# Kernel tuning notes

Hardware: AMD Instinct MI355X
Metric: run time of the kernel (lower is better)

## Reference

```python
import jax, jax.numpy as jnp
import numpy as np

NEG_BIG = -9e15  # matches -9000000000000000.0 in the torch source


def setup_inputs() -> dict:
    key = jax.random.key(0)
    k_h, k_adj, k_W, k_a = jax.random.split(key, 4)
    B, N, F_in, F_out = 8, 2048, 256, 256
    h = jax.random.normal(k_h, (B, N, F_in), dtype=jnp.float32)
    adj = jax.random.randint(k_adj, (B, N, N), 0, 2, dtype=jnp.int32)
    # xavier_uniform with gain=1.414
    gain = 1.414
    lim_W = gain * np.sqrt(6.0 / (F_in + F_out))
    W = jax.random.uniform(k_W, (F_in, F_out), dtype=jnp.float32, minval=-lim_W, maxval=lim_W)
    lim_a = gain * np.sqrt(6.0 / (2 * F_out + 1))
    a = jax.random.uniform(k_a, (2 * F_out, 1), dtype=jnp.float32, minval=-lim_a, maxval=lim_a)
    return {"h": h, "adj": adj, "W": W, "a": a}


def reference(h, adj, W, a):
    # h: [B, N, F_in], adj: [B, N, N], W: [F_in, F_out], a: [2*F_out, 1]
    F_out = W.shape[1]
    Wh = jnp.matmul(h, W)  # [B, N, F_out]
    a1 = a[:F_out, 0]      # [F_out]
    a2 = a[F_out:, 0]      # [F_out]
    # e_ij = Wh_i . a1 + Wh_j . a2  (identical to cat([Wh_i, Wh_j]) @ a)
    e = (Wh @ a1)[:, :, None] + (Wh @ a2)[:, None, :]  # [B, N, N]
    # NOTE: the original torch forward applies no LeakyReLU before softmax.
    masked = jnp.where(adj > 0, e, jnp.float32(NEG_BIG))
    attention = jax.nn.softmax(masked, axis=-1)  # [B, N, N]
    # dropout is a no-op in eval mode (training=False)
    h_prime = jnp.matmul(attention, Wh)  # [B, N, F_out]
    return jax.nn.elu(h_prime)
```

## Files before the change

### kernel.cpp

```cpp
#include <hip/hip_runtime.h>
#include <math.h>

using short8   = __attribute__((ext_vector_type(8))) short;
using floatx4  = __attribute__((ext_vector_type(4))) float;
using ushort4v = __attribute__((ext_vector_type(4))) unsigned short;

#define GLD16(gsrc, ldst) __builtin_amdgcn_global_load_lds( \
    (const __attribute__((address_space(1))) void*)(gsrc),  \
    (__attribute__((address_space(3))) void*)(ldst), 16, 0, 0)

__device__ __forceinline__ unsigned short f2bf(float x) {
  union { float f; unsigned u; } v; v.f = x;
  unsigned r = (v.u + 0x7FFFu + ((v.u >> 16) & 1u)) >> 16;
  return (unsigned short)r;
}
__device__ __forceinline__ float bf2f(unsigned short u) {
  union { unsigned u; float f; } v; v.u = ((unsigned)u) << 16;
  return v.f;
}
__device__ __forceinline__ short8 pack_a(int4 v0, int4 v1) {
  union { uint4 u; short8 s; } r;
  r.u.x = ((unsigned)v0.x | ((unsigned)v0.y << 16)) * 0x3F80u;
  r.u.y = ((unsigned)v0.z | ((unsigned)v0.w << 16)) * 0x3F80u;
  r.u.z = ((unsigned)v1.x | ((unsigned)v1.y << 16)) * 0x3F80u;
  r.u.w = ((unsigned)v1.z | ((unsigned)v1.w << 16)) * 0x3F80u;
  return r.s;
}

__global__ __launch_bounds__(256) void wh_gemm(
    const float* __restrict__ h, const float* __restrict__ W,
    unsigned short* __restrict__ Whb) {
  __shared__ __align__(16) float Al[16][64];
  __shared__ __align__(16) float Bl[16][128];
  const int m0 = blockIdx.x * 64;
  const int n0 = blockIdx.y * 128;
  const int t  = threadIdx.x;
  const int tx = t & 15, ty = t >> 4;
  float acc[4][8];
#pragma unroll
  for (int i = 0; i < 4; ++i)
#pragma unroll
    for (int j = 0; j < 8; ++j) acc[i][j] = 0.0f;

  for (int k0 = 0; k0 < 256; k0 += 16) {
    {
      int m = t & 63, kq = t >> 6;
      float4 v = *(const float4*)&h[(size_t)(m0 + m) * 256 + k0 + kq * 4];
      Al[kq * 4 + 0][m] = v.x; Al[kq * 4 + 1][m] = v.y;
      Al[kq * 4 + 2][m] = v.z; Al[kq * 4 + 3][m] = v.w;
    }
    {
      int n4 = t & 31, kr = t >> 5;
      *(float4*)&Bl[kr][n4 * 4]     = *(const float4*)&W[(size_t)(k0 + kr) * 256 + n0 + n4 * 4];
      *(float4*)&Bl[kr + 8][n4 * 4] = *(const float4*)&W[(size_t)(k0 + kr + 8) * 256 + n0 + n4 * 4];
    }
    __syncthreads();
#pragma unroll
    for (int k = 0; k < 16; ++k) {
      float4 av = *(const float4*)&Al[k][ty * 4];
      float4 b0 = *(const float4*)&Bl[k][tx * 4];
      float4 b1 = *(const float4*)&Bl[k][64 + tx * 4];
      float aa[4] = {av.x, av.y, av.z, av.w};
      float bb[8] = {b0.x, b0.y, b0.z, b0.w, b1.x, b1.y, b1.z, b1.w};
#pragma unroll
      for (int i = 0; i < 4; ++i)
#pragma unroll
        for (int j = 0; j < 8; ++j) acc[i][j] = fmaf(aa[i], bb[j], acc[i][j]);
    }
    __syncthreads();
  }
#pragma unroll
  for (int i = 0; i < 4; ++i) {
    size_t row = (size_t)(m0 + ty * 4 + i);
    ushort4v o0, o1;
#pragma unroll
    for (int j = 0; j < 4; ++j) { o0[j] = f2bf(acc[i][j]); o1[j] = f2bf(acc[i][4 + j]); }
    *(ushort4v*)&Whb[row * 256 + n0 + tx * 4]      = o0;
    *(ushort4v*)&Whb[row * 256 + n0 + 64 + tx * 4] = o1;
  }
}

__global__ __launch_bounds__(256) void g_rows(
    const unsigned short* __restrict__ Whb, const float* __restrict__ a,
    float* __restrict__ g) {
  int row = blockIdx.x * 4 + (threadIdx.x >> 6);
  int L = threadIdx.x & 63;
  ushort4v wv = *(const ushort4v*)&Whb[(size_t)row * 256 + L * 4];
  float4 av = *(const float4*)&a[256 + L * 4];
  float d = bf2f(wv[0]) * av.x + bf2f(wv[1]) * av.y + bf2f(wv[2]) * av.z + bf2f(wv[3]) * av.w;
#pragma unroll
  for (int off = 32; off > 0; off >>= 1) d += __shfl_xor(d, off);
  if (L == 0) g[row] = d;
}

__global__ __launch_bounds__(256) void batch_max(
    const float* __restrict__ g, float* __restrict__ Mb) {
  __shared__ float red[4];
  int b = blockIdx.x, t = threadIdx.x;
  float m = -1e30f;
  for (int i = t; i < 2048; i += 256) m = fmaxf(m, g[(size_t)b * 2048 + i]);
#pragma unroll
  for (int off = 32; off > 0; off >>= 1) m = fmaxf(m, __shfl_xor(m, off));
  if ((t & 63) == 0) red[t >> 6] = m;
  __syncthreads();
  if (t == 0) Mb[b] = fmaxf(fmaxf(red[0], red[1]), fmaxf(red[2], red[3]));
}

__global__ __launch_bounds__(256) void build_bt(
    const unsigned short* __restrict__ Whb, const float* __restrict__ g,
    const float* __restrict__ Mb, unsigned short* __restrict__ Bt) {
  __shared__ __align__(16) unsigned short tile[320 * 64];
  const int blk = blockIdx.x;
  const int b   = blk >> 5;
  const int j0  = (blk & 31) * 64;
  const int kt_base = (blk & 31) * 2;
  const int t   = threadIdx.x;
  const int j   = t & 63;
  const int q0  = t >> 6;
  const int row = b * 2048 + j0 + j;
  const float s = expf(g[row] - Mb[b]);
  for (int q = q0; q < 64; q += 4) {
    ushort4v wv = *(const ushort4v*)&Whb[(size_t)row * 256 + q * 4];
    int c = q * 4;
    tile[(c + 0) * 64 + j] = f2bf(s * bf2f(wv[0]));
    tile[(c + 1) * 64 + j] = f2bf(s * bf2f(wv[1]));
    tile[(c + 2) * 64 + j] = f2bf(s * bf2f(wv[2]));
    tile[(c + 3) * 64 + j] = f2bf(s * bf2f(wv[3]));
  }
  if (q0 == 0) tile[256 * 64 + j] = f2bf(s);
  for (int z = t; z < 63 * 64; z += 256) tile[257 * 64 + z] = 0;
  __syncthreads();
#pragma unroll
  for (int p = 0; p < 10; ++p) {
    int id = t + 256 * p;
    int c = id >> 3, off = id & 7;
    int kt_l = off >> 2, slot = off & 3;
    size_t dst = ((size_t)((b * 64 + kt_base + kt_l) * 320 + c)) * 64 + (slot << 4);
    *(int4*)((char*)Bt + dst) = *(const int4*)&tile[c * 64 + off * 8];
  }
}

__global__ __launch_bounds__(256, 2) void gat_main(
    const int* __restrict__ adj, const unsigned short* __restrict__ Bt,
    float* __restrict__ out) {
  __shared__ __align__(16) char lds[16512];
  const int bid = blockIdx.x;
  const int b   = bid & 7;
  const int rb  = bid >> 3;
  const int i0  = rb * 32;
  const int tid = threadIdx.x;
  const int w   = tid >> 6, L = tid & 63;
  const int fr  = L & 15, kc = L >> 4;

  const char* adjB = (const char*)adj + ((size_t)b * 2048 + i0) * 8192;
  const char* asrc = adjB + (size_t)(w * 8 + (L >> 3)) * 8192 + (((L & 7) ^ (L >> 3)) << 4);
  const char* bsrc = (const char*)Bt + (size_t)b * 1310720
                   + (size_t)(w * 80 + fr) * 64 + (kc << 4);

  char* buf0 = lds;
  char* buf1 = lds + 4096;
  char* buf2 = lds + 8192;
  char* buf3 = lds + 12288;

  floatx4 acc[2][5];
#pragma unroll
  for (int i = 0; i < 2; ++i)
#pragma unroll
    for (int n = 0; n < 5; ++n) acc[i][n] = (floatx4)0.0f;

  short8 pb0[5], pb1[5], pb2[5], pb3[5];

#define STAGEA(TT, BASE) { GLD16(asrc + (size_t)(TT) * 128, (BASE) + w * 1024); }

#define LOADB(TT, SET) {                                  \
    const char* p_ = bsrc + (size_t)(TT) * 20480;         \
    SET[0] = *(const short8*)(p_);                        \
    SET[1] = *(const short8*)(p_ + 1024);                 \
    SET[2] = *(const short8*)(p_ + 2048);                 \
    SET[3] = *(const short8*)(p_ + 3072);                 \
    SET[4] = *(const short8*)(p_ + 4096);                 \
  }

#define COMPUTE(BASE, SET) {                                                     \
    short8 af_[2];                                                               \
    _Pragma("unroll")                                                            \
    for (int mf = 0; mf < 2; ++mf) {                                             \
      const char* ar_ = (BASE) + (mf * 16 + fr) * 128;                           \
      int4 a0_ = *(const int4*)(ar_ + (((2 * kc)     ^ (fr & 7)) << 4));         \
      int4 a1_ = *(const int4*)(ar_ + (((2 * kc + 1) ^ (fr & 7)) << 4));         \
      af_[mf] = pack_a(a0_, a1_);                                                \
    }                                                                            \
    _Pragma("unroll")                                                            \
    for (int nf = 0; nf < 5; ++nf) {                                             \
      acc[0][nf] = __builtin_amdgcn_mfma_f32_16x16x32_bf16(af_[0], SET[nf], acc[0][nf], 0, 0, 0); \
      acc[1][nf] = __builtin_amdgcn_mfma_f32_16x16x32_bf16(af_[1], SET[nf], acc[1][nf], 0, 0, 0); \
    }                                                                            \
  }

#define PH(GATE, CBUF, CSET, STT, SBUF, SSET) {            \
    asm volatile("s_waitcnt vmcnt(" #GATE ")" ::: "memory"); \
    __builtin_amdgcn_s_barrier();                          \
    STAGEA(STT, SBUF);                                     \
    LOADB(STT, SSET);                                      \
    COMPUTE(CBUF, CSET);                                   \
  }

#define PHN(GATE, CBUF, CSET) {                            \
    asm volatile("s_waitcnt vmcnt(" #GATE ")" ::: "memory"); \
    __builtin_amdgcn_s_barrier();                          \
    COMPUTE(CBUF, CSET);                                   \
  }

  STAGEA(0, buf0); LOADB(0, pb0);
  STAGEA(1, buf1); LOADB(1, pb1);
  STAGEA(2, buf2); LOADB(2, pb2);

#pragma unroll 1
  for (int k = 0; k < 15; ++k) {
    int t4 = k * 4;
    PH(12, buf0, pb0, t4 + 3, buf3, pb3);
    PH(12, buf1, pb1, t4 + 4, buf0, pb0);
    PH(12, buf2, pb2, t4 + 5, buf1, pb1);
    PH(12, buf3, pb3, t4 + 6, buf2, pb2);
  }
  PH (12, buf0, pb0, 63, buf3, pb3);
  PHN(12, buf1, pb1);
  PHN(6,  buf2, pb2);
  PHN(0,  buf3, pb3);

  float* denL = (float*)(lds + 16384);
  const int q = L >> 4;
  if (w == 3 && fr == 0) {
#pragma unroll
    for (int mf = 0; mf < 2; ++mf)
#pragma unroll
      for (int jj = 0; jj < 4; ++jj)
        denL[mf * 16 + q * 4 + jj] = acc[mf][1][jj];
  }
  __syncthreads();
  float invd[2][4];
#pragma unroll
  for (int mf = 0; mf < 2; ++mf)
#pragma unroll
    for (int jj = 0; jj < 4; ++jj)
      invd[mf][jj] = 1.0f / denL[mf * 16 + q * 4 + jj];
#pragma unroll
  for (int mf = 0; mf < 2; ++mf) {
#pragma unroll
    for (int nf = 0; nf < 5; ++nf) {
      int col = w * 80 + nf * 16 + fr;
      if (col < 256) {
#pragma unroll
        for (int jj = 0; jj < 4; ++jj) {
          int row = mf * 16 + q * 4 + jj;
          float v = acc[mf][nf][jj] * invd[mf][jj];
          v = (v > 0.0f) ? v : expm1f(v);
          out[((size_t)b * 2048 + i0 + row) * 256 + col] = v;
        }
      }
    }
  }
#undef PH
#undef PHN
#undef COMPUTE
#undef LOADB
#undef STAGEA
}

extern "C" void kernel_launch(void* const* d_in, const int* in_sizes, int n_in,
                              void* d_out, int out_size, void* d_ws, size_t ws_size,
                              hipStream_t stream) {
  const float* h   = (const float*)d_in[0];
  const int*   adj = (const int*)d_in[1];
  const float* W   = (const float*)d_in[2];
  const float* a   = (const float*)d_in[3];
  float* out = (float*)d_out;

  char* ws = (char*)d_ws;
  if (ws_size < 18940160) return;
  unsigned short* Whb = (unsigned short*)ws;
  float* g            = (float*)(ws + 8388608);
  float* Mb           = (float*)(ws + 8454144);
  unsigned short* Bt  = (unsigned short*)(ws + 8454400);

  wh_gemm  <<<dim3(256, 2), 256, 0, stream>>>(h, W, Whb);
  g_rows   <<<4096,        256, 0, stream>>>(Whb, a, g);
  batch_max<<<8,           256, 0, stream>>>(g, Mb);
  build_bt <<<256,         256, 0, stream>>>(Whb, g, Mb, Bt);
  gat_main <<<512,         256, 0, stream>>>(adj, Bt, out);
}
```

Before: 109.7 us.

## Bit-pack adjacency in a pre-pass and enlarge main-kernel row tile

Adds an adj_pack kernel that compresses the int32 adjacency matrix into one bit per entry. The main kernel then loads a 64-row bitmask tile into LDS once and expands the bits into bf16 A fragments in registers, replacing the per-step global-to-LDS staging, its barriers and vmcnt gating. Blocks are enlarged to 512 threads covering 64 rows, with waves split 2x4 over rows and columns. The pack pass still reads the full 134MB adjacency once, so savings depend on removing the staging and sync overhead and on the larger tile reusing B, while the extra launch and lower block count could cost occupancy.

```diff
diff --git a/kernel.cpp b/kernel.cpp
--- a/kernel.cpp
+++ b/kernel.cpp
@@ -4,10 +4,6 @@
 using short8   = __attribute__((ext_vector_type(8))) short;
 using floatx4  = __attribute__((ext_vector_type(4))) float;
 using ushort4v = __attribute__((ext_vector_type(4))) unsigned short;
-
-#define GLD16(gsrc, ldst) __builtin_amdgcn_global_load_lds( \
-    (const __attribute__((address_space(1))) void*)(gsrc),  \
-    (__attribute__((address_space(3))) void*)(ldst), 16, 0, 0)
 
 __device__ __forceinline__ unsigned short f2bf(float x) {
   union { float f; unsigned u; } v; v.f = x;
@@ -18,13 +14,19 @@
   union { unsigned u; float f; } v; v.u = ((unsigned)u) << 16;
   return v.f;
 }
-__device__ __forceinline__ short8 pack_a(int4 v0, int4 v1) {
-  union { uint4 u; short8 s; } r;
-  r.u.x = ((unsigned)v0.x | ((unsigned)v0.y << 16)) * 0x3F80u;
-  r.u.y = ((unsigned)v0.z | ((unsigned)v0.w << 16)) * 0x3F80u;
-  r.u.z = ((unsigned)v1.x | ((unsigned)v1.y << 16)) * 0x3F80u;
-  r.u.w = ((unsigned)v1.z | ((unsigned)v1.w << 16)) * 0x3F80u;
-  return r.s;
+
+__global__ __launch_bounds__(256) void adj_pack(
+    const int* __restrict__ adj, unsigned* __restrict__ pk) {
+  size_t tid = (size_t)blockIdx.x * 256 + threadIdx.x;
+  const int* src = adj + tid * 32;
+  unsigned r = 0;
+#pragma unroll
+  for (int q = 0; q < 8; ++q) {
+    int4 v = *(const int4*)(src + q * 4);
+    r |= ((unsigned)v.x << (4 * q)) | ((unsigned)v.y << (4 * q + 1)) |
+         ((unsigned)v.z << (4 * q + 2)) | ((unsigned)v.w << (4 * q + 3));
+  }
+  pk[tid] = r;
 }
 
 __global__ __launch_bounds__(256) void wh_gemm(
@@ -140,27 +142,33 @@
   }
 }
 
-__global__ __launch_bounds__(256, 2) void gat_main(
-    const int* __restrict__ adj, const unsigned short* __restrict__ Bt,
+__global__ __launch_bounds__(512) void gat_main(
+    const unsigned* __restrict__ pk, const unsigned short* __restrict__ Bt,
     float* __restrict__ out) {
-  __shared__ __align__(16) char lds[16512];
+  __shared__ __align__(16) char lds[64 * 272 + 256];
   const int bid = blockIdx.x;
   const int b   = bid & 7;
   const int rb  = bid >> 3;
-  const int i0  = rb * 32;
+  const int i0  = rb * 64;
   const int tid = threadIdx.x;
   const int w   = tid >> 6, L = tid & 63;
+  const int wm  = w >> 2, wn = w & 3;
   const int fr  = L & 15, kc = L >> 4;
 
-  const char* adjB = (const char*)adj + ((size_t)b * 2048 + i0) * 8192;
-  const char* asrc = adjB + (size_t)(w * 8 + (L >> 3)) * 8192 + (((L & 7) ^ (L >> 3)) << 4);
+  {
+    int r = tid >> 3, seg = tid & 7;
+    const char* src = (const char*)pk + ((size_t)(b * 2048 + i0 + r) * 256 + seg * 32);
+    char* dst = lds + r * 272 + seg * 32;
+    *(int4*)(dst)      = *(const int4*)(src);
+    *(int4*)(dst + 16) = *(const int4*)(src + 16);
+  }
+  __syncthreads();
+
   const char* bsrc = (const char*)Bt + (size_t)b * 1310720
-                   + (size_t)(w * 80 + fr) * 64 + (kc << 4);
-
-  char* buf0 = lds;
-  char* buf1 = lds + 4096;
-  char* buf2 = lds + 8192;
-  char* buf3 = lds + 12288;
+                   + (size_t)(wn * 80 + fr) * 64 + (kc << 4);
+  const char* arow0 = lds + (wm * 32 + fr) * 272;
+  const char* arow1 = arow0 + 16 * 272;
+  const int   ksh   = kc * 8;
 
   floatx4 acc[2][5];
 #pragma unroll
@@ -168,9 +176,7 @@
 #pragma unroll
     for (int n = 0; n < 5; ++n) acc[i][n] = (floatx4)0.0f;
 
-  short8 pb0[5], pb1[5], pb2[5], pb3[5];
-
-#define STAGEA(TT, BASE) { GLD16(asrc + (size_t)(TT) * 128, (BASE) + w * 1024); }
+  short8 s0[5], s1[5], s2[5], s3[5];
 
 #define LOADB(TT, SET) {                                  \
     const char* p_ = bsrc + (size_t)(TT) * 20480;         \
@@ -181,61 +187,50 @@
     SET[4] = *(const short8*)(p_ + 4096);                 \
   }
 
-#define COMPUTE(BASE, SET) {                                                     \
-    short8 af_[2];                                                               \
-    _Pragma("unroll")                                                            \
-    for (int mf = 0; mf < 2; ++mf) {                                             \
-      const char* ar_ = (BASE) + (mf * 16 + fr) * 128;                           \
-      int4 a0_ = *(const int4*)(ar_ + (((2 * kc)     ^ (fr & 7)) << 4));         \
-      int4 a1_ = *(const int4*)(ar_ + (((2 * kc + 1) ^ (fr & 7)) << 4));         \
-      af_[mf] = pack_a(a0_, a1_);                                                \
-    }                                                                            \
+#define AFRAG(AROW, TT, DST) {                            \
+    unsigned word_ = *(const unsigned*)((AROW) + (TT) * 4); \
+    unsigned x_ = (word_ >> ksh) & 0xFFu;                 \
+    unsigned y_ = x_ | (x_ << 15);                        \
+    union { unsigned u[4]; short8 s; } c_;                \
+    c_.u[0] = (y_        & 0x10001u) * 0x3F80u;           \
+    c_.u[1] = ((y_ >> 2) & 0x10001u) * 0x3F80u;           \
+    c_.u[2] = ((y_ >> 4) & 0x10001u) * 0x3F80u;           \
+    c_.u[3] = ((y_ >> 6) & 0x10001u) * 0x3F80u;           \
+    DST = c_.s;                                           \
+  }
+
+#define COMPUTE(TT, SET) {                                                       \
+    short8 af0_, af1_;                                                           \
+    AFRAG(arow0, TT, af0_);                                                      \
+    AFRAG(arow1, TT, af1_);                                                      \
     _Pragma("unroll")                                                            \
     for (int nf = 0; nf < 5; ++nf) {                                             \
-      acc[0][nf] = __builtin_amdgcn_mfma_f32_16x16x32_bf16(af_[0], SET[nf], acc[0][nf], 0, 0, 0); \
-      acc[1][nf] = __builtin_amdgcn_mfma_f32_16x16x32_bf16(af_[1], SET[nf], acc[1][nf], 0, 0, 0); \
+      acc[0][nf] = __builtin_amdgcn_mfma_f32_16x16x32_bf16(af0_, SET[nf], acc[0][nf], 0, 0, 0); \
+      acc[1][nf] = __builtin_amdgcn_mfma_f32_16x16x32_bf16(af1_, SET[nf], acc[1][nf], 0, 0, 0); \
     }                                                                            \
   }
 
-#define PH(GATE, CBUF, CSET, STT, SBUF, SSET) {            \
-    asm volatile("s_waitcnt vmcnt(" #GATE ")" ::: "memory"); \
-    __builtin_amdgcn_s_barrier();                          \
-    STAGEA(STT, SBUF);                                     \
-    LOADB(STT, SSET);                                      \
-    COMPUTE(CBUF, CSET);                                   \
-  }
-
-#define PHN(GATE, CBUF, CSET) {                            \
-    asm volatile("s_waitcnt vmcnt(" #GATE ")" ::: "memory"); \
-    __builtin_amdgcn_s_barrier();                          \
-    COMPUTE(CBUF, CSET);                                   \
-  }
-
-  STAGEA(0, buf0); LOADB(0, pb0);
-  STAGEA(1, buf1); LOADB(1, pb1);
-  STAGEA(2, buf2); LOADB(2, pb2);
+  LOADB(0, s0); LOADB(1, s1); LOADB(2, s2);
 
 #pragma unroll 1
   for (int k = 0; k < 15; ++k) {
     int t4 = k * 4;
-    PH(12, buf0, pb0, t4 + 3, buf3, pb3);
-    PH(12, buf1, pb1, t4 + 4, buf0, pb0);
-    PH(12, buf2, pb2, t4 + 5, buf1, pb1);
-    PH(12, buf3, pb3, t4 + 6, buf2, pb2);
-  }
-  PH (12, buf0, pb0, 63, buf3, pb3);
-  PHN(12, buf1, pb1);
-  PHN(6,  buf2, pb2);
-  PHN(0,  buf3, pb3);
-
-  float* denL = (float*)(lds + 16384);
+    LOADB(t4 + 3, s3); COMPUTE(t4 + 0, s0);
+    LOADB(t4 + 4, s0); COMPUTE(t4 + 1, s1);
+    LOADB(t4 + 5, s1); COMPUTE(t4 + 2, s2);
+    LOADB(t4 + 6, s2); COMPUTE(t4 + 3, s3);
+  }
+  LOADB(63, s3);
+  COMPUTE(60, s0); COMPUTE(61, s1); COMPUTE(62, s2); COMPUTE(63, s3);
+
+  float* denL = (float*)(lds + 64 * 272);
   const int q = L >> 4;
-  if (w == 3 && fr == 0) {
+  if (wn == 3 && fr == 0) {
 #pragma unroll
     for (int mf = 0; mf < 2; ++mf)
 #pragma unroll
       for (int jj = 0; jj < 4; ++jj)
-        denL[mf * 16 + q * 4 + jj] = acc[mf][1][jj];
+        denL[wm * 32 + mf * 16 + q * 4 + jj] = acc[mf][1][jj];
   }
   __syncthreads();
   float invd[2][4];
@@ -243,16 +238,16 @@
   for (int mf = 0; mf < 2; ++mf)
 #pragma unroll
     for (int jj = 0; jj < 4; ++jj)
-      invd[mf][jj] = 1.0f / denL[mf * 16 + q * 4 + jj];
+      invd[mf][jj] = 1.0f / denL[wm * 32 + mf * 16 + q * 4 + jj];
 #pragma unroll
   for (int mf = 0; mf < 2; ++mf) {
 #pragma unroll
     for (int nf = 0; nf < 5; ++nf) {
-      int col = w * 80 + nf * 16 + fr;
+      int col = wn * 80 + nf * 16 + fr;
       if (col < 256) {
 #pragma unroll
         for (int jj = 0; jj < 4; ++jj) {
-          int row = mf * 16 + q * 4 + jj;
+          int row = wm * 32 + mf * 16 + q * 4 + jj;
           float v = acc[mf][nf][jj] * invd[mf][jj];
           v = (v > 0.0f) ? v : expm1f(v);
           out[((size_t)b * 2048 + i0 + row) * 256 + col] = v;
@@ -260,11 +255,9 @@
       }
     }
   }
-#undef PH
-#undef PHN
 #undef COMPUTE
+#undef AFRAG
 #undef LOADB
-#undef STAGEA
 }
 
 extern "C" void kernel_launch(void* const* d_in, const int* in_sizes, int n_in,
@@ -277,15 +270,17 @@
   float* out = (float*)d_out;
 
   char* ws = (char*)d_ws;
-  if (ws_size < 18940160) return;
+  if (ws_size < 23134464) return;
   unsigned short* Whb = (unsigned short*)ws;
   float* g            = (float*)(ws + 8388608);
   float* Mb           = (float*)(ws + 8454144);
   unsigned short* Bt  = (unsigned short*)(ws + 8454400);
-
+  unsigned* pk        = (unsigned*)(ws + 18940160);
+
+  adj_pack <<<4096,        256, 0, stream>>>(adj, pk);
   wh_gemm  <<<dim3(256, 2), 256, 0, stream>>>(h, W, Whb);
   g_rows   <<<4096,        256, 0, stream>>>(Whb, a, g);
   batch_max<<<8,           256, 0, stream>>>(g, Mb);
   build_bt <<<256,         256, 0, stream>>>(Whb, g, Mb, Bt);
-  gat_main <<<512,         256, 0, stream>>>(adj, Bt, out);
-}
+  gat_main <<<256,         512, 0, stream>>>(pk, Bt, out);
+}
```

Measured after the change: 113.5 us. 1.03x slower.
